# Kernel tuning notes

Hardware: AMD Instinct MI355X
Metric: run time of the kernel (lower is better)

The kernel has to match this reference:

```python
import jax, jax.numpy as jnp
import numpy as np


def setup_inputs() -> dict:
    key = jax.random.key(0)
    k1, k2 = jax.random.split(key)
    B, H, S = 4, 16, 1024  # batch, heads, seq_len (attention logits [B,H,S,S])
    x = jax.random.normal(k1, (B, H, S, S), dtype=jnp.float32)
    v = jax.random.normal(k2, (B, H, 1, S), dtype=jnp.float32)  # per-key value weights
    return {"x": x, "v": v}


def reference(x, v):
    # Forward of the wrapped rule: softmax over the last (key) dim, then
    # elementwise multiplication with the value tensor (broadcast over queries).
    # The chunked vmap in the original is purely a memory-management detail of
    # its custom backward; the forward math is softmax(x) * v.
    return jax.nn.softmax(x, axis=-1) * v
```

## Files before the change

kernel.cpp:

```cpp
#include <hip/hip_runtime.h>


#define SEQ 1024
#define WAVES_PER_BLOCK 4

typedef float vf4 __attribute__((ext_vector_type(4)));

__global__ __launch_bounds__(256) void softmax_mul_kernel(
    const float* __restrict__ x,
    const float* __restrict__ v,
    float* __restrict__ out,
    int npairs) {
  const int wave = threadIdx.x >> 6;
  const int lane = threadIdx.x & 63;
  const int pair = blockIdx.x * WAVES_PER_BLOCK + wave;
  if (pair >= npairs) return;

  const size_t row0 = (size_t)pair * 2;
  const vf4* __restrict__ x4 = (const vf4*)(x + row0 * SEQ);
  vf4* __restrict__ o4 = (vf4*)(out + row0 * SEQ);
  const vf4* __restrict__ v4 = (const vf4*)(v + (row0 >> 10) * SEQ);

  vf4 a[4], b[4], vv[4];
#pragma unroll
  for (int j = 0; j < 4; ++j) a[j] = __builtin_nontemporal_load(&x4[lane + 64 * j]);
#pragma unroll
  for (int j = 0; j < 4; ++j) b[j] = __builtin_nontemporal_load(&x4[256 + lane + 64 * j]);
#pragma unroll
  for (int j = 0; j < 4; ++j) vv[j] = v4[lane + 64 * j];

  float ma = -INFINITY, mb = -INFINITY;
#pragma unroll
  for (int j = 0; j < 4; ++j) {
    ma = fmaxf(ma, fmaxf(fmaxf(a[j].x, a[j].y), fmaxf(a[j].z, a[j].w)));
    mb = fmaxf(mb, fmaxf(fmaxf(b[j].x, b[j].y), fmaxf(b[j].z, b[j].w)));
  }
#pragma unroll
  for (int off = 32; off > 0; off >>= 1) {
    ma = fmaxf(ma, __shfl_xor(ma, off, 64));
    mb = fmaxf(mb, __shfl_xor(mb, off, 64));
  }

  float sa = 0.f, sb = 0.f;
#pragma unroll
  for (int j = 0; j < 4; ++j) {
    a[j].x = __expf(a[j].x - ma); a[j].y = __expf(a[j].y - ma);
    a[j].z = __expf(a[j].z - ma); a[j].w = __expf(a[j].w - ma);
    b[j].x = __expf(b[j].x - mb); b[j].y = __expf(b[j].y - mb);
    b[j].z = __expf(b[j].z - mb); b[j].w = __expf(b[j].w - mb);
    sa += (a[j].x + a[j].y) + (a[j].z + a[j].w);
    sb += (b[j].x + b[j].y) + (b[j].z + b[j].w);
  }
#pragma unroll
  for (int off = 32; off > 0; off >>= 1) {
    sa += __shfl_xor(sa, off, 64);
    sb += __shfl_xor(sb, off, 64);
  }
  const float ia = 1.0f / sa;
  const float ib = 1.0f / sb;

#pragma unroll
  for (int j = 0; j < 4; ++j) {
    vf4 oa, ob;
    oa.x = a[j].x * ia * vv[j].x; oa.y = a[j].y * ia * vv[j].y;
    oa.z = a[j].z * ia * vv[j].z; oa.w = a[j].w * ia * vv[j].w;
    ob.x = b[j].x * ib * vv[j].x; ob.y = b[j].y * ib * vv[j].y;
    ob.z = b[j].z * ib * vv[j].z; ob.w = b[j].w * ib * vv[j].w;
    __builtin_nontemporal_store(oa, &o4[lane + 64 * j]);
    __builtin_nontemporal_store(ob, &o4[256 + lane + 64 * j]);
  }
}

extern "C" void kernel_launch(void* const* d_in, const int* in_sizes, int n_in,
                              void* d_out, int out_size, void* d_ws, size_t ws_size,
                              hipStream_t stream) {
  const float* x = (const float*)d_in[0];
  const float* v = (const float*)d_in[1];
  float* out = (float*)d_out;
  const int rows = in_sizes[0] / SEQ;
  const int npairs = rows / 2;
  const int grid = (npairs + WAVES_PER_BLOCK - 1) / WAVES_PER_BLOCK;
  softmax_mul_kernel<<<grid, 256, 0, stream>>>(x, v, out, npairs);
}
```

Before: 416.5 us.

## Use online-softmax merge in wave reduction with native exp2 and rcp

Drops the separate wave-wide max reduction. Each lane uses its local max, and the max and sum are merged together in one butterfly shuffle pass with online-softmax rescaling. The exponentials become native exp2 with a fused multiply-add by log2e, and the final scale uses a fast reciprocal folded into the value multiply. This removes one shuffle-reduction round of latency but adds exp2 work in the reduction and a per-lane correction factor. The kernel is memory-bound, so the effect is likely small.

```diff
diff --git a/kernel.cpp b/kernel.cpp
--- a/kernel.cpp
+++ b/kernel.cpp
@@ -3,6 +3,7 @@
 
 #define SEQ 1024
 #define WAVES_PER_BLOCK 4
+#define LOG2E 1.44269504088896340736f
 
 typedef float vf4 __attribute__((ext_vector_type(4)));
 
@@ -35,37 +36,55 @@
     ma = fmaxf(ma, fmaxf(fmaxf(a[j].x, a[j].y), fmaxf(a[j].z, a[j].w)));
     mb = fmaxf(mb, fmaxf(fmaxf(b[j].x, b[j].y), fmaxf(b[j].z, b[j].w)));
   }
-#pragma unroll
-  for (int off = 32; off > 0; off >>= 1) {
-    ma = fmaxf(ma, __shfl_xor(ma, off, 64));
-    mb = fmaxf(mb, __shfl_xor(mb, off, 64));
-  }
+  float m2a = ma * LOG2E;
+  float m2b = mb * LOG2E;
 
   float sa = 0.f, sb = 0.f;
 #pragma unroll
   for (int j = 0; j < 4; ++j) {
-    a[j].x = __expf(a[j].x - ma); a[j].y = __expf(a[j].y - ma);
-    a[j].z = __expf(a[j].z - ma); a[j].w = __expf(a[j].w - ma);
-    b[j].x = __expf(b[j].x - mb); b[j].y = __expf(b[j].y - mb);
-    b[j].z = __expf(b[j].z - mb); b[j].w = __expf(b[j].w - mb);
+    a[j].x = __builtin_amdgcn_exp2f(__builtin_fmaf(a[j].x, LOG2E, -m2a));
+    a[j].y = __builtin_amdgcn_exp2f(__builtin_fmaf(a[j].y, LOG2E, -m2a));
+    a[j].z = __builtin_amdgcn_exp2f(__builtin_fmaf(a[j].z, LOG2E, -m2a));
+    a[j].w = __builtin_amdgcn_exp2f(__builtin_fmaf(a[j].w, LOG2E, -m2a));
+    b[j].x = __builtin_amdgcn_exp2f(__builtin_fmaf(b[j].x, LOG2E, -m2b));
+    b[j].y = __builtin_amdgcn_exp2f(__builtin_fmaf(b[j].y, LOG2E, -m2b));
+    b[j].z = __builtin_amdgcn_exp2f(__builtin_fmaf(b[j].z, LOG2E, -m2b));
+    b[j].w = __builtin_amdgcn_exp2f(__builtin_fmaf(b[j].w, LOG2E, -m2b));
     sa += (a[j].x + a[j].y) + (a[j].z + a[j].w);
     sb += (b[j].x + b[j].y) + (b[j].z + b[j].w);
   }
+
+  const float lm2a = m2a, lm2b = m2b;
 #pragma unroll
   for (int off = 32; off > 0; off >>= 1) {
-    sa += __shfl_xor(sa, off, 64);
-    sb += __shfl_xor(sb, off, 64);
+    const float oma = __shfl_xor(m2a, off, 64);
+    const float osa = __shfl_xor(sa, off, 64);
+    const float omb = __shfl_xor(m2b, off, 64);
+    const float osb = __shfl_xor(sb, off, 64);
+    const float nma = fmaxf(m2a, oma);
+    const float nmb = fmaxf(m2b, omb);
+    sa = sa * __builtin_amdgcn_exp2f(m2a - nma)
+       + osa * __builtin_amdgcn_exp2f(oma - nma);
+    sb = sb * __builtin_amdgcn_exp2f(m2b - nmb)
+       + osb * __builtin_amdgcn_exp2f(omb - nmb);
+    m2a = nma;
+    m2b = nmb;
   }
-  const float ia = 1.0f / sa;
-  const float ib = 1.0f / sb;
+
+  const float fa = __builtin_amdgcn_exp2f(lm2a - m2a) * __builtin_amdgcn_rcpf(sa);
+  const float fb = __builtin_amdgcn_exp2f(lm2b - m2b) * __builtin_amdgcn_rcpf(sb);
 
 #pragma unroll
   for (int j = 0; j < 4; ++j) {
-    vf4 oa, ob;
-    oa.x = a[j].x * ia * vv[j].x; oa.y = a[j].y * ia * vv[j].y;
-    oa.z = a[j].z * ia * vv[j].z; oa.w = a[j].w * ia * vv[j].w;
-    ob.x = b[j].x * ib * vv[j].x; ob.y = b[j].y * ib * vv[j].y;
-    ob.z = b[j].z * ib * vv[j].z; ob.w = b[j].w * ib * vv[j].w;
+    vf4 fva, fvb, oa, ob;
+    fva.x = fa * vv[j].x; fva.y = fa * vv[j].y;
+    fva.z = fa * vv[j].z; fva.w = fa * vv[j].w;
+    fvb.x = fb * vv[j].x; fvb.y = fb * vv[j].y;
+    fvb.z = fb * vv[j].z; fvb.w = fb * vv[j].w;
+    oa.x = a[j].x * fva.x; oa.y = a[j].y * fva.y;
+    oa.z = a[j].z * fva.z; oa.w = a[j].w * fva.w;
+    ob.x = b[j].x * fvb.x; ob.y = b[j].y * fvb.y;
+    ob.z = b[j].z * fvb.z; ob.w = b[j].w * fvb.w;
     __builtin_nontemporal_store(oa, &o4[lane + 64 * j]);
     __builtin_nontemporal_store(ob, &o4[256 + lane + 64 * j]);
   }
```

Result: no change. 415.1 us (-0.3%).
